# Kernel optimization log

Hardware: AMD Instinct MI355X
Metric: run time of the kernel (lower is better)

The kernel has to match this reference:

```python
import math
import jax, jax.numpy as jnp
import numpy as np

B = 65536
EMBED = 256
COND = 256
TIME = 128
HID = 256
E = 8
RHID = 128
IN_DIM = EMBED + TIME + COND  # 640


def setup_inputs() -> dict:
    key = jax.random.key(0)
    ks = jax.random.split(key, 20)
    s = 0.02
    inp = {
        "z_t": jax.random.normal(ks[0], (B, EMBED), jnp.float32),
        "t": jax.random.uniform(ks[1], (B, 1), jnp.float32),
        "cond": jax.random.normal(ks[2], (B, COND), jnp.float32),
        # time embedding proj (Linear(time,time) -> SiLU -> Linear(time,time))
        "tW1": jax.random.normal(ks[3], (TIME, TIME), jnp.float32) * s,
        "tb1": jnp.zeros((TIME,), jnp.float32),
        "tW2": jax.random.normal(ks[4], (TIME, TIME), jnp.float32) * s,
        "tb2": jnp.zeros((TIME,), jnp.float32),
        # stacked expert weights [E, in, out]
        "eW1": jax.random.normal(ks[5], (E, IN_DIM, HID), jnp.float32) * s,
        "eb1": jnp.zeros((E, HID), jnp.float32),
        "eW2": jax.random.normal(ks[6], (E, HID, HID), jnp.float32) * s,
        "eb2": jnp.zeros((E, HID), jnp.float32),
        "eW3": jax.random.normal(ks[7], (E, HID, EMBED), jnp.float32) * s,
        "eb3": jnp.zeros((E, EMBED), jnp.float32),
        # router
        "rW1": jax.random.normal(ks[8], (IN_DIM, RHID), jnp.float32) * s,
        "rb1": jnp.zeros((RHID,), jnp.float32),
        "rW2": jax.random.normal(ks[9], (RHID, E), jnp.float32) * s,
        "rb2": jnp.zeros((E,), jnp.float32),
    }
    return inp


def _time_embedding(t, tW1, tb1, tW2, tb2):
    half = TIME // 2  # 64
    scale = -math.log(10000.0) / (half - 1)
    freqs = jnp.exp(jnp.arange(half, dtype=t.dtype) * scale)[None, :]  # [1, half]
    angles = t * freqs  # [B, half]
    emb = jnp.concatenate([jnp.sin(angles), jnp.cos(angles)], axis=-1)  # [B, TIME]
    h = jax.nn.silu(emb @ tW1 + tb1)
    return h @ tW2 + tb2


def reference(z_t, t, cond, tW1, tb1, tW2, tb2, eW1, eb1, eW2, eb2, eW3, eb3, rW1, rb1, rW2, rb2):
    time_emb = _time_embedding(t, tW1, tb1, tW2, tb2)
    x = jnp.concatenate([z_t, time_emb, cond], axis=-1)  # [B, IN_DIM]
    # dense MoE: all experts via batched GEMMs (dropout=0 -> identity)
    h1 = jax.nn.silu(jnp.einsum('bi,eih->beh', x, eW1) + eb1)      # [B,E,HID]
    h2 = jax.nn.silu(jnp.einsum('beh,ehk->bek', h1, eW2) + eb2)    # [B,E,HID]
    expert_out = jnp.einsum('beh,ehd->bed', h2, eW3) + eb3         # [B,E,EMBED]
    # router softmax gate
    rh = jax.nn.silu(x @ rW1 + rb1)
    gate = jax.nn.softmax(rh @ rW2 + rb2, axis=-1)                 # [B,E]
    velocity = jnp.einsum('be,bed->bd', gate, expert_out)          # [B,EMBED]
    return velocity, gate
```

## Files before the change

### kernel.cpp

```cpp
#include <hip/hip_runtime.h>

typedef __attribute__((ext_vector_type(8))) short bf16x8;
typedef __attribute__((ext_vector_type(4))) float f32x4;

#define NB_ROWS 65536
#define D_EMBED 256
#define D_HID   256
#define N_EXP   8
#define D_RHID  128
#define D_IN    640
#define D_H1    2048

#define KSTR 72
#define HSTR 264

static __device__ __forceinline__ ushort f2bf(float f) {
  union { float f; unsigned u; } v; v.f = f;
  unsigned r = v.u + 0x7fffu + ((v.u >> 16) & 1u);
  return (ushort)(r >> 16);
}
static __device__ __forceinline__ float bf2f(ushort h) {
  union { unsigned u; float f; } v; v.u = ((unsigned)h) << 16;
  return v.f;
}
static __device__ __forceinline__ float silu_f(float x) {
  return x / (1.0f + __expf(-x));
}

static __device__ __forceinline__ int kswz(int r, int c) {
  return r * 64 + ((((c) >> 3) ^ (r & 7)) << 3) + ((c) & 7);
}

__global__ void prep_transpose(const float* __restrict__ src, ushort* __restrict__ dst,
                               int R, int C, int total) {
  int idx = blockIdx.x * 256 + threadIdx.x;
  if (idx >= total) return;
  int rc = R * C;
  int m = idx / rc;
  int rem = idx - m * rc;
  int r = rem / C;
  int c = rem - r * C;
  dst[m * rc + c * R + r] = f2bf(src[idx]);
}

static __device__ __forceinline__ void stA128s(const ushort* __restrict__ src, int ld,
                                               int kt, ushort* dst, int tid) {
  uint4 v[2];
  #pragma unroll
  for (int c = 0; c < 2; ++c) {
    int f = c * 8192 + tid * 16;
    int r = f >> 7, ce = (f & 127) >> 1;
    v[c] = *(const uint4*)&src[(size_t)r * ld + kt + ce];
  }
  #pragma unroll
  for (int c = 0; c < 2; ++c) {
    int f = c * 8192 + tid * 16;
    int r = f >> 7, ce = (f & 127) >> 1;
    *(uint4*)&dst[kswz(r, ce)] = v[c];
  }
}
static __device__ __forceinline__ void stB256s(const ushort* __restrict__ src, int ld,
                                               int kt, ushort* dst, int tid) {
  uint4 v[4];
  #pragma unroll
  for (int c = 0; c < 4; ++c) {
    int f = c * 8192 + tid * 16;
    int r = f >> 7, ce = (f & 127) >> 1;
    v[c] = *(const uint4*)&src[(size_t)r * ld + kt + ce];
  }
  #pragma unroll
  for (int c = 0; c < 4; ++c) {
    int f = c * 8192 + tid * 16;
    int r = f >> 7, ce = (f & 127) >> 1;
    *(uint4*)&dst[kswz(r, ce)] = v[c];
  }
}
static __device__ __forceinline__ void stageA128_256(const ushort* __restrict__ src, int ld,
                                                     int kt, ushort* dst, int tid) {
  uint4 v[4];
  #pragma unroll
  for (int c = 0; c < 4; ++c) {
    int f = c * 4096 + tid * 16;
    int r = f >> 7, ce = (f & 127) >> 1;
    v[c] = *(const uint4*)&src[(size_t)r * ld + kt + ce];
  }
  #pragma unroll
  for (int c = 0; c < 4; ++c) {
    int f = c * 4096 + tid * 16;
    int r = f >> 7, ce = (f & 127) >> 1;
    *(uint4*)&dst[r * KSTR + ce] = v[c];
  }
}

__global__ __launch_bounds__(512) void time_x_kernel(
    const float* __restrict__ zt, const float* __restrict__ tin,
    const float* __restrict__ cond,
    const ushort* __restrict__ tw1t, const ushort* __restrict__ tw2t,
    const float* __restrict__ tb1, const float* __restrict__ tb2,
    ushort* __restrict__ x) {
  __shared__ __align__(16) ushort sE[128 * 136];
  __shared__ float sFreq[64];
  __shared__ float sB1[128];
  __shared__ float sB2[128];

  const int tid = threadIdx.x;
  const int row0 = blockIdx.x * 128;

  for (int ch = tid; ch < 128 * 64; ch += 512) {
    int r = ch >> 6;
    int c4 = (ch & 63) << 2;
    size_t grow = (size_t)(row0 + r);
    float4 zv = *(const float4*)&zt[grow * 256 + c4];
    ushort4 o; o.x = f2bf(zv.x); o.y = f2bf(zv.y); o.z = f2bf(zv.z); o.w = f2bf(zv.w);
    *(ushort4*)&x[grow * 640 + c4] = o;
    float4 cv = *(const float4*)&cond[grow * 256 + c4];
    ushort4 o2; o2.x = f2bf(cv.x); o2.y = f2bf(cv.y); o2.z = f2bf(cv.z); o2.w = f2bf(cv.w);
    *(ushort4*)&x[grow * 640 + 384 + c4] = o2;
  }

  if (tid < 64) sFreq[tid] = __expf((float)tid * (-9.210340371976184f / 63.0f));
  if (tid < 128) { sB1[tid] = tb1[tid]; sB2[tid] = tb2[tid]; }
  __syncthreads();

  {
    int r = tid >> 2;
    int qd = tid & 3;
    float tv = tin[row0 + r];
    int half = qd >> 1;
    int cbase = (qd & 1) * 32;
    ushort* er = &sE[r * 136 + half * 64 + cbase];
    #pragma unroll
    for (int c = 0; c < 32; ++c) {
      float a = tv * sFreq[cbase + c];
      float v = half ? __cosf(a) : __sinf(a);
      er[c] = f2bf(v);
    }
  }
  __syncthreads();

  const int l = tid & 63;
  const int w = tid >> 6;
  const int wm = w >> 1;
  const int wn = w & 1;
  const int lr = l & 15;
  const int lk = (l >> 4) * 8;
  const int q4 = (l >> 4) * 4;

  f32x4 acc[2][4] = {};
  #pragma unroll
  for (int kk = 0; kk < 4; ++kk) {
    int kb = kk * 32 + lk;
    bf16x8 av[2], bv[4];
    #pragma unroll
    for (int mf = 0; mf < 2; ++mf)
      av[mf] = *(const bf16x8*)&sE[(wm * 32 + mf * 16 + lr) * 136 + kb];
    #pragma unroll
    for (int nf = 0; nf < 4; ++nf)
      bv[nf] = *(const bf16x8*)&tw1t[(size_t)(wn * 64 + nf * 16 + lr) * 128 + kb];
    #pragma unroll
    for (int mf = 0; mf < 2; ++mf)
      #pragma unroll
      for (int nf = 0; nf < 4; ++nf)
        acc[mf][nf] = __builtin_amdgcn_mfma_f32_16x16x32_bf16(av[mf], bv[nf], acc[mf][nf], 0, 0, 0);
  }
  __syncthreads();
  #pragma unroll
  for (int mf = 0; mf < 2; ++mf)
    #pragma unroll
    for (int nf = 0; nf < 4; ++nf) {
      int cc = wn * 64 + nf * 16 + lr;
      #pragma unroll
      for (int rg = 0; rg < 4; ++rg) {
        int rr = wm * 32 + mf * 16 + q4 + rg;
        sE[rr * 136 + cc] = f2bf(silu_f(acc[mf][nf][rg] + sB1[cc]));
      }
    }
  __syncthreads();

  f32x4 acc2[2][4] = {};
  #pragma unroll
  for (int kk = 0; kk < 4; ++kk) {
    int kb = kk * 32 + lk;
    bf16x8 av[2], bv[4];
    #pragma unroll
    for (int mf = 0; mf < 2; ++mf)
      av[mf] = *(const bf16x8*)&sE[(wm * 32 + mf * 16 + lr) * 136 + kb];
    #pragma unroll
    for (int nf = 0; nf < 4; ++nf)
      bv[nf] = *(const bf16x8*)&tw2t[(size_t)(wn * 64 + nf * 16 + lr) * 128 + kb];
    #pragma unroll
    for (int mf = 0; mf < 2; ++mf)
      #pragma unroll
      for (int nf = 0; nf < 4; ++nf)
        acc2[mf][nf] = __builtin_amdgcn_mfma_f32_16x16x32_bf16(av[mf], bv[nf], acc2[mf][nf], 0, 0, 0);
  }
  #pragma unroll
  for (int mf = 0; mf < 2; ++mf)
    #pragma unroll
    for (int nf = 0; nf < 4; ++nf) {
      int cc = wn * 64 + nf * 16 + lr;
      #pragma unroll
      for (int rg = 0; rg < 4; ++rg) {
        int rr = wm * 32 + mf * 16 + q4 + rg;
        x[(size_t)(row0 + rr) * 640 + 256 + cc] = f2bf(acc2[mf][nf][rg] + sB2[cc]);
      }
    }
}

__global__ __launch_bounds__(256) void router_kernel(
    const ushort* __restrict__ xb, const ushort* __restrict__ rw1t,
    const float* __restrict__ rb1, const float* __restrict__ rW2,
    const float* __restrict__ rb2, float* __restrict__ gatef,
    float* __restrict__ gateo) {
  __shared__ __align__(16) ushort smA[128 * KSTR];
  __shared__ __align__(16) ushort smB[128 * KSTR];
  __shared__ __align__(16) ushort rhbuf[128 * 136];
  __shared__ float sW2[128 * 8];

  const int tid = threadIdx.x;
  const int row0 = blockIdx.x * 128;
  for (int i = tid; i < 1024; i += 256) sW2[i] = rW2[i];

  const int l = tid & 63;
  const int w = tid >> 6;
  const int wm = w >> 1, wn = w & 1;
  const int lr = l & 15, lk = (l >> 4) * 8, q4 = (l >> 4) * 4;
  const ushort* xrow = xb + (size_t)row0 * 640;

  f32x4 acc[4][4] = {};
  for (int kt = 0; kt < 640; kt += 64) {
    stageA128_256(xrow, 640, kt, smA, tid);
    stageA128_256(rw1t, 640, kt, smB, tid);
    __syncthreads();
    #pragma unroll
    for (int kk = 0; kk < 2; ++kk) {
      int kb = kk * 32 + lk;
      bf16x8 av[4], bv[4];
      #pragma unroll
      for (int mf = 0; mf < 4; ++mf)
        av[mf] = *(const bf16x8*)&smA[(wm * 64 + mf * 16 + lr) * KSTR + kb];
      #pragma unroll
      for (int nf = 0; nf < 4; ++nf)
        bv[nf] = *(const bf16x8*)&smB[(wn * 64 + nf * 16 + lr) * KSTR + kb];
      #pragma unroll
      for (int mf = 0; mf < 4; ++mf)
        #pragma unroll
        for (int nf = 0; nf < 4; ++nf)
          acc[mf][nf] = __builtin_amdgcn_mfma_f32_16x16x32_bf16(av[mf], bv[nf], acc[mf][nf], 0, 0, 0);
    }
    __syncthreads();
  }
  #pragma unroll
  for (int nf = 0; nf < 4; ++nf) {
    int cc = wn * 64 + nf * 16 + lr;
    float b1v = rb1[cc];
    #pragma unroll
    for (int mf = 0; mf < 4; ++mf)
      #pragma unroll
      for (int rg = 0; rg < 4; ++rg) {
        int rr = wm * 64 + mf * 16 + q4 + rg;
        rhbuf[rr * 136 + cc] = f2bf(silu_f(acc[mf][nf][rg] + b1v));
      }
  }
  __syncthreads();

  if (tid < 128) {
    float a[8];
    #pragma unroll
    for (int e = 0; e < 8; ++e) a[e] = rb2[e];
    #pragma unroll
    for (int i8 = 0; i8 < 16; ++i8) {
      bf16x8 hv = *(const bf16x8*)&rhbuf[tid * 136 + i8 * 8];
      #pragma unroll
      for (int j = 0; j < 8; ++j) {
        float h = bf2f((ushort)hv[j]);
        const float* wrow = &sW2[(i8 * 8 + j) * 8];
        #pragma unroll
        for (int e = 0; e < 8; ++e) a[e] += h * wrow[e];
      }
    }
    float mx = a[0];
    #pragma unroll
    for (int e = 1; e < 8; ++e) mx = fmaxf(mx, a[e]);
    float s = 0.f, ex[8];
    #pragma unroll
    for (int e = 0; e < 8; ++e) { ex[e] = __expf(a[e] - mx); s += ex[e]; }
    float inv = 1.f / s;
    size_t b = (size_t)(row0 + tid);
    #pragma unroll
    for (int e = 0; e < 8; ++e) {
      float g = ex[e] * inv;
      gatef[b * 8 + e] = g;
      gateo[b * 8 + e] = g;
    }
  }
}

__global__ __launch_bounds__(512) void moe_h1_kernel(
    const ushort* __restrict__ xb, const ushort* __restrict__ w1t,
    const float* __restrict__ eb1, ushort* __restrict__ hg) {
  __shared__ __align__(16) ushort smA[128 * 64];
  __shared__ __align__(16) ushort smB[256 * 64];

  const int tid = threadIdx.x;
  int flat = blockIdx.x;
  int sid = (flat & 7) * 512 + (flat >> 3);
  const int rb = sid >> 3;
  const int e  = sid & 7;
  const int row0 = rb * 128;

  const int l = tid & 63;
  const int w = tid >> 6;
  const int wm = w >> 2, wn = w & 3;
  const int lr = l & 15, lk = (l >> 4) * 8, q4 = (l >> 4) * 4;

  const ushort* xrow = xb + (size_t)row0 * 640;
  const ushort* W1 = w1t + (size_t)e * (256 * 640);

  f32x4 acc[4][4] = {};
  for (int kt = 0; kt < 640; kt += 64) {
    stA128s(xrow, 640, kt, smA, tid);
    stB256s(W1, 640, kt, smB, tid);
    __syncthreads();
    #pragma unroll
    for (int kk = 0; kk < 2; ++kk) {
      int kb = kk * 32 + lk;
      bf16x8 av[4], bv[4];
      #pragma unroll
      for (int mf = 0; mf < 4; ++mf)
        av[mf] = *(const bf16x8*)&smA[kswz(wm * 64 + mf * 16 + lr, kb)];
      #pragma unroll
      for (int nf = 0; nf < 4; ++nf)
        bv[nf] = *(const bf16x8*)&smB[kswz(wn * 64 + nf * 16 + lr, kb)];
      #pragma unroll
      for (int mf = 0; mf < 4; ++mf)
        #pragma unroll
        for (int nf = 0; nf < 4; ++nf)
          acc[mf][nf] = __builtin_amdgcn_mfma_f32_16x16x32_bf16(av[mf], bv[nf], acc[mf][nf], 0, 0, 0);
    }
    __syncthreads();
  }
  #pragma unroll
  for (int nf = 0; nf < 4; ++nf) {
    int cc = wn * 64 + nf * 16 + lr;
    float b1v = eb1[e * 256 + cc];
    #pragma unroll
    for (int mf = 0; mf < 4; ++mf)
      #pragma unroll
      for (int rg = 0; rg < 4; ++rg) {
        int rr = wm * 64 + mf * 16 + q4 + rg;
        hg[(size_t)(row0 + rr) * D_H1 + e * 256 + cc] = f2bf(silu_f(acc[mf][nf][rg] + b1v));
      }
  }
}

__global__ __launch_bounds__(512) void moe_h2_kernel(
    ushort* __restrict__ hg, const ushort* __restrict__ w2t,
    const float* __restrict__ eb2, const float* __restrict__ gatef) {
  __shared__ __align__(16) ushort smA[128 * 64];
  __shared__ __align__(16) ushort smB[256 * 64];
  __shared__ float sGate[128];

  const int tid = threadIdx.x;
  int flat = blockIdx.x;
  int sid = (flat & 7) * 512 + (flat >> 3);
  const int rb = sid >> 3;
  const int e  = sid & 7;
  const int row0 = rb * 128;

  const int l = tid & 63;
  const int w = tid >> 6;
  const int wm = w >> 2, wn = w & 3;
  const int lr = l & 15, lk = (l >> 4) * 8, q4 = (l >> 4) * 4;

  if (tid < 128) sGate[tid] = gatef[(size_t)(row0 + tid) * 8 + e];

  ushort* hrow = hg + (size_t)row0 * D_H1 + e * 256;
  const ushort* W2 = w2t + (size_t)e * (256 * 256);

  f32x4 acc[4][4] = {};
  for (int kt = 0; kt < 256; kt += 64) {
    stA128s(hrow, D_H1, kt, smA, tid);
    stB256s(W2, 256, kt, smB, tid);
    __syncthreads();
    #pragma unroll
    for (int kk = 0; kk < 2; ++kk) {
      int kb = kk * 32 + lk;
      bf16x8 av[4], bv[4];
      #pragma unroll
      for (int mf = 0; mf < 4; ++mf)
        av[mf] = *(const bf16x8*)&smA[kswz(wm * 64 + mf * 16 + lr, kb)];
      #pragma unroll
      for (int nf = 0; nf < 4; ++nf)
        bv[nf] = *(const bf16x8*)&smB[kswz(wn * 64 + nf * 16 + lr, kb)];
      #pragma unroll
      for (int mf = 0; mf < 4; ++mf)
        #pragma unroll
        for (int nf = 0; nf < 4; ++nf)
          acc[mf][nf] = __builtin_amdgcn_mfma_f32_16x16x32_bf16(av[mf], bv[nf], acc[mf][nf], 0, 0, 0);
    }
    __syncthreads();
  }
  #pragma unroll
  for (int nf = 0; nf < 4; ++nf) {
    int cc = wn * 64 + nf * 16 + lr;
    float b2v = eb2[e * 256 + cc];
    #pragma unroll
    for (int mf = 0; mf < 4; ++mf)
      #pragma unroll
      for (int rg = 0; rg < 4; ++rg) {
        int rr = wm * 64 + mf * 16 + q4 + rg;
        hrow[(size_t)rr * D_H1 + cc] = f2bf(silu_f(acc[mf][nf][rg] + b2v) * sGate[rr]);
      }
  }
}

__global__ __launch_bounds__(512) void moe_vel_kernel(
    const ushort* __restrict__ hg, const ushort* __restrict__ w3t,
    const float* __restrict__ eb3, const float* __restrict__ gatef,
    float* __restrict__ velout) {
  __shared__ __align__(16) ushort smA[128 * 64];
  __shared__ __align__(16) ushort smB[256 * 64];
  __shared__ float sGate[128 * 8];

  const int tid = threadIdx.x;
  const int row0 = blockIdx.x * 128;
  const int l = tid & 63;
  const int w = tid >> 6;
  const int wm = w >> 2, wn = w & 3;
  const int lr = l & 15, lk = (l >> 4) * 8, q4 = (l >> 4) * 4;

  for (int i = tid; i < 1024; i += 512) sGate[i] = gatef[(size_t)row0 * 8 + i];

  const ushort* hrow = hg + (size_t)row0 * D_H1;
  f32x4 vacc[4][4] = {};
  __syncthreads();

  for (int kt = 0; kt < 2048; kt += 64) {
    const int e = kt >> 8;
    stA128s(hrow, D_H1, kt, smA, tid);
    stB256s(w3t + (size_t)e * (256 * 256), 256, kt & 255, smB, tid);
    __syncthreads();
    #pragma unroll
    for (int kk = 0; kk < 2; ++kk) {
      int kb = kk * 32 + lk;
      bf16x8 av[4], bv[4];
      #pragma unroll
      for (int mf = 0; mf < 4; ++mf)
        av[mf] = *(const bf16x8*)&smA[kswz(wm * 64 + mf * 16 + lr, kb)];
      #pragma unroll
      for (int nf = 0; nf < 4; ++nf)
        bv[nf] = *(const bf16x8*)&smB[kswz(wn * 64 + nf * 16 + lr, kb)];
      #pragma unroll
      for (int mf = 0; mf < 4; ++mf)
        #pragma unroll
        for (int nf = 0; nf < 4; ++nf)
          vacc[mf][nf] = __builtin_amdgcn_mfma_f32_16x16x32_bf16(av[mf], bv[nf], vacc[mf][nf], 0, 0, 0);
    }
    __syncthreads();
  }

  float* eL = (float*)smB;
  for (int i = tid; i < 2048; i += 512) eL[i] = eb3[i];
  __syncthreads();
  #pragma unroll
  for (int mf = 0; mf < 4; ++mf)
    #pragma unroll
    for (int rg = 0; rg < 4; ++rg) {
      int rr = wm * 64 + mf * 16 + q4 + rg;
      const float* gp = &sGate[rr * 8];
      #pragma unroll
      for (int nf = 0; nf < 4; ++nf) {
        int cc = wn * 64 + nf * 16 + lr;
        float bsum = 0.f;
        #pragma unroll
        for (int ee = 0; ee < 8; ++ee) bsum += gp[ee] * eL[ee * 256 + cc];
        velout[(size_t)(row0 + rr) * D_EMBED + cc] = vacc[mf][nf][rg] + bsum;
      }
    }
}

__global__ __launch_bounds__(512) void moe_fused_kernel(
    const ushort* __restrict__ xb, const ushort* __restrict__ w1t,
    const ushort* __restrict__ w2t, const ushort* __restrict__ w3t,
    const float* __restrict__ eb1, const float* __restrict__ eb2,
    const float* __restrict__ eb3, const float* __restrict__ gatef,
    float* __restrict__ velout) {
  __shared__ __align__(16) ushort smA[128 * 64];
  __shared__ __align__(16) ushort smB[256 * 64];
  __shared__ __align__(16) ushort hbuf[128 * HSTR];
  __shared__ float sGate[128 * 8];
  __shared__ float sEb3[8 * 256];

  const int tid = threadIdx.x;
  const int row0 = blockIdx.x * 128;
  const int l = tid & 63;
  const int w = tid >> 6;
  const int wm = w >> 2, wn = w & 3;
  const int lr = l & 15, lk = (l >> 4) * 8, q4 = (l >> 4) * 4;

  for (int i = tid; i < 1024; i += 512) sGate[i] = gatef[(size_t)row0 * 8 + i];
  for (int i = tid; i < 2048; i += 512) sEb3[i] = eb3[i];

  const ushort* xrow = xb + (size_t)row0 * 640;
  f32x4 vacc[4][4] = {};
  __syncthreads();

  for (int e = 0; e < 8; ++e) {
    const ushort* W1 = w1t + (size_t)e * (256 * 640);
    const ushort* W2 = w2t + (size_t)e * (256 * 256);
    const ushort* W3 = w3t + (size_t)e * (256 * 256);

    f32x4 acc[4][4] = {};
    for (int kt = 0; kt < 640; kt += 64) {
      stA128s(xrow, 640, kt, smA, tid);
      stB256s(W1, 640, kt, smB, tid);
      __syncthreads();
      #pragma unroll
      for (int kk = 0; kk < 2; ++kk) {
        int kb = kk * 32 + lk;
        bf16x8 av[4], bv[4];
        #pragma unroll
        for (int mf = 0; mf < 4; ++mf)
          av[mf] = *(const bf16x8*)&smA[kswz(wm * 64 + mf * 16 + lr, kb)];
        #pragma unroll
        for (int nf = 0; nf < 4; ++nf)
          bv[nf] = *(const bf16x8*)&smB[kswz(wn * 64 + nf * 16 + lr, kb)];
        #pragma unroll
        for (int mf = 0; mf < 4; ++mf)
          #pragma unroll
          for (int nf = 0; nf < 4; ++nf)
            acc[mf][nf] = __builtin_amdgcn_mfma_f32_16x16x32_bf16(av[mf], bv[nf], acc[mf][nf], 0, 0, 0);
      }
      __syncthreads();
    }
    #pragma unroll
    for (int nf = 0; nf < 4; ++nf) {
      int cc = wn * 64 + nf * 16 + lr;
      float b1v = eb1[e * 256 + cc];
      #pragma unroll
      for (int mf = 0; mf < 4; ++mf)
        #pragma unroll
        for (int rg = 0; rg < 4; ++rg) {
          int rr = wm * 64 + mf * 16 + q4 + rg;
          hbuf[rr * HSTR + cc] = f2bf(silu_f(acc[mf][nf][rg] + b1v));
        }
    }
    __syncthreads();

    #pragma unroll
    for (int mf = 0; mf < 4; ++mf)
      #pragma unroll
      for (int nf = 0; nf < 4; ++nf)
        acc[mf][nf] = (f32x4){0.f, 0.f, 0.f, 0.f};
    for (int kt = 0; kt < 256; kt += 64) {
      stB256s(W2, 256, kt, smB, tid);
      __syncthreads();
      #pragma unroll
      for (int kk = 0; kk < 2; ++kk) {
        int kbl = kk * 32 + lk;
        int kbh = kt + kbl;
        bf16x8 av[4], bv[4];
        #pragma unroll
        for (int mf = 0; mf < 4; ++mf)
          av[mf] = *(const bf16x8*)&hbuf[(wm * 64 + mf * 16 + lr) * HSTR + kbh];
        #pragma unroll
        for (int nf = 0; nf < 4; ++nf)
          bv[nf] = *(const bf16x8*)&smB[kswz(wn * 64 + nf * 16 + lr, kbl)];
        #pragma unroll
        for (int mf = 0; mf < 4; ++mf)
          #pragma unroll
          for (int nf = 0; nf < 4; ++nf)
            acc[mf][nf] = __builtin_amdgcn_mfma_f32_16x16x32_bf16(av[mf], bv[nf], acc[mf][nf], 0, 0, 0);
      }
      __syncthreads();
    }
    #pragma unroll
    for (int nf = 0; nf < 4; ++nf) {
      int cc = wn * 64 + nf * 16 + lr;
      float b2v = eb2[e * 256 + cc];
      #pragma unroll
      for (int mf = 0; mf < 4; ++mf)
        #pragma unroll
        for (int rg = 0; rg < 4; ++rg) {
          int rr = wm * 64 + mf * 16 + q4 + rg;
          float gv = sGate[rr * 8 + e];
          hbuf[rr * HSTR + cc] = f2bf(silu_f(acc[mf][nf][rg] + b2v) * gv);
        }
    }
    __syncthreads();

    for (int kt = 0; kt < 256; kt += 64) {
      stB256s(W3, 256, kt, smB, tid);
      __syncthreads();
      #pragma unroll
      for (int kk = 0; kk < 2; ++kk) {
        int kbl = kk * 32 + lk;
        int kbh = kt + kbl;
        bf16x8 av[4], bv[4];
        #pragma unroll
        for (int mf = 0; mf < 4; ++mf)
          av[mf] = *(const bf16x8*)&hbuf[(wm * 64 + mf * 16 + lr) * HSTR + kbh];
        #pragma unroll
        for (int nf = 0; nf < 4; ++nf)
          bv[nf] = *(const bf16x8*)&smB[kswz(wn * 64 + nf * 16 + lr, kbl)];
        #pragma unroll
        for (int mf = 0; mf < 4; ++mf)
          #pragma unroll
          for (int nf = 0; nf < 4; ++nf)
            vacc[mf][nf] = __builtin_amdgcn_mfma_f32_16x16x32_bf16(av[mf], bv[nf], vacc[mf][nf], 0, 0, 0);
      }
      __syncthreads();
    }
  }

  #pragma unroll
  for (int mf = 0; mf < 4; ++mf)
    #pragma unroll
    for (int rg = 0; rg < 4; ++rg) {
      int rr = wm * 64 + mf * 16 + q4 + rg;
      const float* gp = &sGate[rr * 8];
      #pragma unroll
      for (int nf = 0; nf < 4; ++nf) {
        int cc = wn * 64 + nf * 16 + lr;
        float bsum = 0.f;
        #pragma unroll
        for (int ee = 0; ee < 8; ++ee) bsum += gp[ee] * sEb3[ee * 256 + cc];
        velout[(size_t)(row0 + rr) * D_EMBED + cc] = vacc[mf][nf][rg] + bsum;
      }
    }
}

extern "C" void kernel_launch(void* const* d_in, const int* in_sizes, int n_in,
                              void* d_out, int out_size, void* d_ws, size_t ws_size,
                              hipStream_t stream) {
  const float* zt   = (const float*)d_in[0];
  const float* tin  = (const float*)d_in[1];
  const float* cond = (const float*)d_in[2];
  const float* tW1  = (const float*)d_in[3];
  const float* tb1  = (const float*)d_in[4];
  const float* tW2  = (const float*)d_in[5];
  const float* tb2  = (const float*)d_in[6];
  const float* eW1  = (const float*)d_in[7];
  const float* eb1  = (const float*)d_in[8];
  const float* eW2  = (const float*)d_in[9];
  const float* eb2  = (const float*)d_in[10];
  const float* eW3  = (const float*)d_in[11];
  const float* eb3  = (const float*)d_in[12];
  const float* rW1  = (const float*)d_in[13];
  const float* rb1  = (const float*)d_in[14];
  const float* rW2  = (const float*)d_in[15];
  const float* rb2  = (const float*)d_in[16];

  char* wp = (char*)d_ws;
  ushort* xb    = (ushort*)wp; wp += (size_t)NB_ROWS * D_IN * 2;
  float*  gatef = (float*)wp;  wp += (size_t)NB_ROWS * 8 * 4;
  ushort* w1t   = (ushort*)wp; wp += (size_t)N_EXP * D_HID * D_IN * 2;
  ushort* w2t   = (ushort*)wp; wp += (size_t)N_EXP * D_HID * D_HID * 2;
  ushort* w3t   = (ushort*)wp; wp += (size_t)N_EXP * D_HID * D_EMBED * 2;
  ushort* rw1t  = (ushort*)wp; wp += (size_t)D_RHID * D_IN * 2;
  ushort* tw1t  = (ushort*)wp; wp += (size_t)128 * 128 * 2;
  ushort* tw2t  = (ushort*)wp; wp += (size_t)128 * 128 * 2;
  ushort* hg    = (ushort*)wp; wp += (size_t)NB_ROWS * D_H1 * 2;
  size_t need_big = (size_t)(wp - (char*)d_ws);

  float* velout  = (float*)d_out;
  float* gateout = velout + (size_t)NB_ROWS * D_EMBED;

  {
    int tot;
    tot = 128 * 128;
    prep_transpose<<<(tot + 255) / 256, 256, 0, stream>>>(tW1, tw1t, 128, 128, tot);
    prep_transpose<<<(tot + 255) / 256, 256, 0, stream>>>(tW2, tw2t, 128, 128, tot);
    tot = D_IN * D_RHID;
    prep_transpose<<<(tot + 255) / 256, 256, 0, stream>>>(rW1, rw1t, D_IN, D_RHID, tot);
    tot = N_EXP * D_IN * D_HID;
    prep_transpose<<<(tot + 255) / 256, 256, 0, stream>>>(eW1, w1t, D_IN, D_HID, tot);
    tot = N_EXP * D_HID * D_HID;
    prep_transpose<<<(tot + 255) / 256, 256, 0, stream>>>(eW2, w2t, D_HID, D_HID, tot);
    tot = N_EXP * D_HID * D_EMBED;
    prep_transpose<<<(tot + 255) / 256, 256, 0, stream>>>(eW3, w3t, D_HID, D_EMBED, tot);
  }

  time_x_kernel<<<512, 512, 0, stream>>>(zt, tin, cond, tw1t, tw2t, tb1, tb2, xb);
  router_kernel<<<512, 256, 0, stream>>>(xb, rw1t, rb1, rW2, rb2, gatef, gateout);

  if (ws_size >= need_big) {
    moe_h1_kernel<<<4096, 512, 0, stream>>>(xb, w1t, eb1, hg);
    moe_h2_kernel<<<4096, 512, 0, stream>>>(hg, w2t, eb2, gatef);
    moe_vel_kernel<<<512, 512, 0, stream>>>(hg, w3t, eb3, gatef, velout);
  } else {
    moe_fused_kernel<<<512, 512, 0, stream>>>(xb, w1t, w2t, w3t,
                                              eb1, eb2, eb3, gatef, velout);
  }
}
```

Before: 660.1 us.

## Chunk MoE rows to fit workspace and retile velocity kernel to 64x128

The three-kernel MoE path now processes rows in chunks sized to the available workspace, so the intermediate hidden buffer can shrink and stay closer to cache rather than needing the full batch allocation. The velocity kernel is retiled from 128x256 tiles with 512 threads to 64x128 tiles with 256 threads, giving four times as many workgroups so more CUs are busy during the long K=2048 reduction. Each workgroup in that kernel now rereads the A tile for both column halves, adding some traffic, and chunking adds kernel launches.

```diff
diff --git a/kernel.cpp b/kernel.cpp
--- a/kernel.cpp
+++ b/kernel.cpp
@@ -75,6 +75,38 @@
     *(uint4*)&dst[kswz(r, ce)] = v[c];
   }
 }
+static __device__ __forceinline__ void stA64_256s(const ushort* __restrict__ src, int ld,
+                                                  int kt, ushort* dst, int tid) {
+  uint4 v[2];
+  #pragma unroll
+  for (int c = 0; c < 2; ++c) {
+    int f = c * 4096 + tid * 16;
+    int r = f >> 7, ce = (f & 127) >> 1;
+    v[c] = *(const uint4*)&src[(size_t)r * ld + kt + ce];
+  }
+  #pragma unroll
+  for (int c = 0; c < 2; ++c) {
+    int f = c * 4096 + tid * 16;
+    int r = f >> 7, ce = (f & 127) >> 1;
+    *(uint4*)&dst[kswz(r, ce)] = v[c];
+  }
+}
+static __device__ __forceinline__ void stB128_256s(const ushort* __restrict__ src, int ld,
+                                                   int kt, ushort* dst, int tid) {
+  uint4 v[4];
+  #pragma unroll
+  for (int c = 0; c < 4; ++c) {
+    int f = c * 4096 + tid * 16;
+    int r = f >> 7, ce = (f & 127) >> 1;
+    v[c] = *(const uint4*)&src[(size_t)r * ld + kt + ce];
+  }
+  #pragma unroll
+  for (int c = 0; c < 4; ++c) {
+    int f = c * 4096 + tid * 16;
+    int r = f >> 7, ce = (f & 127) >> 1;
+    *(uint4*)&dst[kswz(r, ce)] = v[c];
+  }
+}
 static __device__ __forceinline__ void stageA128_256(const ushort* __restrict__ src, int ld,
                                                      int kt, ushort* dst, int tid) {
   uint4 v[4];
@@ -298,23 +330,24 @@
 
 __global__ __launch_bounds__(512) void moe_h1_kernel(
     const ushort* __restrict__ xb, const ushort* __restrict__ w1t,
-    const float* __restrict__ eb1, ushort* __restrict__ hg) {
+    const float* __restrict__ eb1, ushort* __restrict__ hg, int row_base) {
   __shared__ __align__(16) ushort smA[128 * 64];
   __shared__ __align__(16) ushort smB[256 * 64];
 
   const int tid = threadIdx.x;
+  int nwg = gridDim.x;
   int flat = blockIdx.x;
-  int sid = (flat & 7) * 512 + (flat >> 3);
+  int sid = (flat & 7) * (nwg >> 3) + (flat >> 3);
   const int rb = sid >> 3;
   const int e  = sid & 7;
-  const int row0 = rb * 128;
+  const int lrow0 = rb * 128;
 
   const int l = tid & 63;
   const int w = tid >> 6;
   const int wm = w >> 2, wn = w & 3;
   const int lr = l & 15, lk = (l >> 4) * 8, q4 = (l >> 4) * 4;
 
-  const ushort* xrow = xb + (size_t)row0 * 640;
+  const ushort* xrow = xb + (size_t)(row_base + lrow0) * 640;
   const ushort* W1 = w1t + (size_t)e * (256 * 640);
 
   f32x4 acc[4][4] = {};
@@ -349,33 +382,34 @@
       #pragma unroll
       for (int rg = 0; rg < 4; ++rg) {
         int rr = wm * 64 + mf * 16 + q4 + rg;
-        hg[(size_t)(row0 + rr) * D_H1 + e * 256 + cc] = f2bf(silu_f(acc[mf][nf][rg] + b1v));
+        hg[(size_t)(lrow0 + rr) * D_H1 + e * 256 + cc] = f2bf(silu_f(acc[mf][nf][rg] + b1v));
       }
   }
 }
 
 __global__ __launch_bounds__(512) void moe_h2_kernel(
     ushort* __restrict__ hg, const ushort* __restrict__ w2t,
-    const float* __restrict__ eb2, const float* __restrict__ gatef) {
+    const float* __restrict__ eb2, const float* __restrict__ gatef, int row_base) {
   __shared__ __align__(16) ushort smA[128 * 64];
   __shared__ __align__(16) ushort smB[256 * 64];
   __shared__ float sGate[128];
 
   const int tid = threadIdx.x;
+  int nwg = gridDim.x;
   int flat = blockIdx.x;
-  int sid = (flat & 7) * 512 + (flat >> 3);
+  int sid = (flat & 7) * (nwg >> 3) + (flat >> 3);
   const int rb = sid >> 3;
   const int e  = sid & 7;
-  const int row0 = rb * 128;
+  const int lrow0 = rb * 128;
 
   const int l = tid & 63;
   const int w = tid >> 6;
   const int wm = w >> 2, wn = w & 3;
   const int lr = l & 15, lk = (l >> 4) * 8, q4 = (l >> 4) * 4;
 
-  if (tid < 128) sGate[tid] = gatef[(size_t)(row0 + tid) * 8 + e];
-
-  ushort* hrow = hg + (size_t)row0 * D_H1 + e * 256;
+  if (tid < 128) sGate[tid] = gatef[(size_t)(row_base + lrow0 + tid) * 8 + e];
+
+  ushort* hrow = hg + (size_t)lrow0 * D_H1 + e * 256;
   const ushort* W2 = w2t + (size_t)e * (256 * 256);
 
   f32x4 acc[4][4] = {};
@@ -415,44 +449,56 @@
   }
 }
 
-__global__ __launch_bounds__(512) void moe_vel_kernel(
+__global__ __launch_bounds__(256) void moe_vel_kernel(
     const ushort* __restrict__ hg, const ushort* __restrict__ w3t,
     const float* __restrict__ eb3, const float* __restrict__ gatef,
-    float* __restrict__ velout) {
-  __shared__ __align__(16) ushort smA[128 * 64];
-  __shared__ __align__(16) ushort smB[256 * 64];
-  __shared__ float sGate[128 * 8];
+    float* __restrict__ velout, int row_base) {
+  __shared__ __align__(16) ushort smA[64 * 64];
+  __shared__ __align__(16) ushort smB[128 * 64];
+  __shared__ float sGate[64 * 8];
+  __shared__ float sEb3[8 * 128];
 
   const int tid = threadIdx.x;
-  const int row0 = blockIdx.x * 128;
+  int nwg = gridDim.x;
+  int flat = blockIdx.x;
+  int sid = (flat & 7) * (nwg >> 3) + (flat >> 3);
+  const int rb = sid >> 1;
+  const int nb = sid & 1;
+  const int lrow0 = rb * 64;
+  const int col0 = nb * 128;
+
   const int l = tid & 63;
   const int w = tid >> 6;
-  const int wm = w >> 2, wn = w & 3;
+  const int wm = w >> 1, wn = w & 1;
   const int lr = l & 15, lk = (l >> 4) * 8, q4 = (l >> 4) * 4;
 
-  for (int i = tid; i < 1024; i += 512) sGate[i] = gatef[(size_t)row0 * 8 + i];
-
-  const ushort* hrow = hg + (size_t)row0 * D_H1;
-  f32x4 vacc[4][4] = {};
+  for (int i = tid; i < 512; i += 256) sGate[i] = gatef[(size_t)(row_base + lrow0) * 8 + i];
+  for (int i = tid; i < 1024; i += 256) {
+    int ee = i >> 7, c = i & 127;
+    sEb3[i] = eb3[ee * 256 + col0 + c];
+  }
+
+  const ushort* hrow = hg + (size_t)lrow0 * D_H1;
+  f32x4 vacc[2][4] = {};
   __syncthreads();
 
   for (int kt = 0; kt < 2048; kt += 64) {
     const int e = kt >> 8;
-    stA128s(hrow, D_H1, kt, smA, tid);
-    stB256s(w3t + (size_t)e * (256 * 256), 256, kt & 255, smB, tid);
+    stA64_256s(hrow, D_H1, kt, smA, tid);
+    stB128_256s(w3t + (size_t)e * (256 * 256) + (size_t)col0 * 256, 256, kt & 255, smB, tid);
     __syncthreads();
     #pragma unroll
     for (int kk = 0; kk < 2; ++kk) {
       int kb = kk * 32 + lk;
-      bf16x8 av[4], bv[4];
-      #pragma unroll
-      for (int mf = 0; mf < 4; ++mf)
-        av[mf] = *(const bf16x8*)&smA[kswz(wm * 64 + mf * 16 + lr, kb)];
+      bf16x8 av[2], bv[4];
+      #pragma unroll
+      for (int mf = 0; mf < 2; ++mf)
+        av[mf] = *(const bf16x8*)&smA[kswz(wm * 32 + mf * 16 + lr, kb)];
       #pragma unroll
       for (int nf = 0; nf < 4; ++nf)
         bv[nf] = *(const bf16x8*)&smB[kswz(wn * 64 + nf * 16 + lr, kb)];
       #pragma unroll
-      for (int mf = 0; mf < 4; ++mf)
+      for (int mf = 0; mf < 2; ++mf)
         #pragma unroll
         for (int nf = 0; nf < 4; ++nf)
           vacc[mf][nf] = __builtin_amdgcn_mfma_f32_16x16x32_bf16(av[mf], bv[nf], vacc[mf][nf], 0, 0, 0);
@@ -460,22 +506,19 @@
     __syncthreads();
   }
 
-  float* eL = (float*)smB;
-  for (int i = tid; i < 2048; i += 512) eL[i] = eb3[i];
-  __syncthreads();
-  #pragma unroll
-  for (int mf = 0; mf < 4; ++mf)
+  #pragma unroll
+  for (int mf = 0; mf < 2; ++mf)
     #pragma unroll
     for (int rg = 0; rg < 4; ++rg) {
-      int rr = wm * 64 + mf * 16 + q4 + rg;
+      int rr = wm * 32 + mf * 16 + q4 + rg;
       const float* gp = &sGate[rr * 8];
       #pragma unroll
       for (int nf = 0; nf < 4; ++nf) {
         int cc = wn * 64 + nf * 16 + lr;
         float bsum = 0.f;
         #pragma unroll
-        for (int ee = 0; ee < 8; ++ee) bsum += gp[ee] * eL[ee * 256 + cc];
-        velout[(size_t)(row0 + rr) * D_EMBED + cc] = vacc[mf][nf][rg] + bsum;
+        for (int ee = 0; ee < 8; ++ee) bsum += gp[ee] * sEb3[ee * 128 + cc];
+        velout[(size_t)(row_base + lrow0 + rr) * D_EMBED + col0 + cc] = vacc[mf][nf][rg] + bsum;
       }
     }
 }
@@ -661,8 +704,13 @@
   ushort* rw1t  = (ushort*)wp; wp += (size_t)D_RHID * D_IN * 2;
   ushort* tw1t  = (ushort*)wp; wp += (size_t)128 * 128 * 2;
   ushort* tw2t  = (ushort*)wp; wp += (size_t)128 * 128 * 2;
-  ushort* hg    = (ushort*)wp; wp += (size_t)NB_ROWS * D_H1 * 2;
-  size_t need_big = (size_t)(wp - (char*)d_ws);
+  ushort* hg    = (ushort*)wp;
+  size_t base = (size_t)(wp - (char*)d_ws);
+
+  int CH = 0;
+  for (int cand = NB_ROWS; cand >= 8192; cand >>= 1) {
+    if (base + (size_t)cand * D_H1 * 2 <= ws_size) { CH = cand; break; }
+  }
 
   float* velout  = (float*)d_out;
   float* gateout = velout + (size_t)NB_ROWS * D_EMBED;
@@ -685,10 +733,12 @@
   time_x_kernel<<<512, 512, 0, stream>>>(zt, tin, cond, tw1t, tw2t, tb1, tb2, xb);
   router_kernel<<<512, 256, 0, stream>>>(xb, rw1t, rb1, rW2, rb2, gatef, gateout);
 
-  if (ws_size >= need_big) {
-    moe_h1_kernel<<<4096, 512, 0, stream>>>(xb, w1t, eb1, hg);
-    moe_h2_kernel<<<4096, 512, 0, stream>>>(hg, w2t, eb2, gatef);
-    moe_vel_kernel<<<512, 512, 0, stream>>>(hg, w3t, eb3, gatef, velout);
+  if (CH > 0) {
+    for (int r0 = 0; r0 < NB_ROWS; r0 += CH) {
+      moe_h1_kernel<<<(CH / 128) * 8, 512, 0, stream>>>(xb, w1t, eb1, hg, r0);
+      moe_h2_kernel<<<(CH / 128) * 8, 512, 0, stream>>>(hg, w2t, eb2, gatef, r0);
+      moe_vel_kernel<<<(CH / 64) * 2, 256, 0, stream>>>(hg, w3t, eb3, gatef, velout, r0);
+    }
   } else {
     moe_fused_kernel<<<512, 512, 0, stream>>>(xb, w1t, w2t, w3t,
                                               eb1, eb2, eb3, gatef, velout);
```

After: 670.8 us. Within noise of the previous version (+1.6%).

## Load expert weights via direct global-to-LDS with pre-swizzled layout; chunk rows

Applied to the files above, without the earlier changes.

Expert weight matrices are now pre-swizzled during the transpose prep so the B tiles can be copied straight into LDS with global_load_lds, skipping the register round trip in the split h1/h2/vel kernels. The row dimension is split into chunks sized to the available workspace, so the intermediate hidden buffer can be smaller, and the vel kernel gains a block-index remap. The fused fallback switches to a linear LDS store to match the new weight layout. This relies on the swizzle produced by the prep step matching the one used for reads, and adds extra launches when chunking is needed.

```diff
diff --git a/kernel.cpp b/kernel.cpp
--- a/kernel.cpp
+++ b/kernel.cpp
@@ -42,7 +42,31 @@
   int c = rem - r * C;
   dst[m * rc + c * R + r] = f2bf(src[idx]);
 }
-
+__global__ void prep_transpose_swz(const float* __restrict__ src, ushort* __restrict__ dst,
+                                   int R, int C, int total) {
+  int idx = blockIdx.x * 256 + threadIdx.x;
+  if (idx >= total) return;
+  int rc = R * C;
+  int m = idx / rc;
+  int rem = idx - m * rc;
+  int r = rem / C;
+  int c = rem - r * C;
+  int p = (r & ~63) + (((((r >> 3) & 7) ^ (c & 7)) << 3) | (r & 7));
+  dst[m * rc + c * R + p] = f2bf(src[idx]);
+}
+
+static __device__ __forceinline__ void glB256_512(const ushort* __restrict__ src, int ld,
+                                                  int kt, ushort* dst, int tid, int w) {
+  #pragma unroll
+  for (int c = 0; c < 4; ++c) {
+    int f = c * 8192 + tid * 16;
+    int r = f >> 7, ce = (f & 127) >> 1;
+    __builtin_amdgcn_global_load_lds(
+        (const __attribute__((address_space(1))) void*)(src + (size_t)r * ld + kt + ce),
+        (__attribute__((address_space(3))) void*)(dst + ((c * 8192 + w * 1024) >> 1)),
+        16, 0, 0);
+  }
+}
 static __device__ __forceinline__ void stA128s(const ushort* __restrict__ src, int ld,
                                                int kt, ushort* dst, int tid) {
   uint4 v[2];
@@ -59,8 +83,8 @@
     *(uint4*)&dst[kswz(r, ce)] = v[c];
   }
 }
-static __device__ __forceinline__ void stB256s(const ushort* __restrict__ src, int ld,
-                                               int kt, ushort* dst, int tid) {
+static __device__ __forceinline__ void stB256lin(const ushort* __restrict__ src, int ld,
+                                                 int kt, ushort* dst, int tid) {
   uint4 v[4];
   #pragma unroll
   for (int c = 0; c < 4; ++c) {
@@ -72,7 +96,7 @@
   for (int c = 0; c < 4; ++c) {
     int f = c * 8192 + tid * 16;
     int r = f >> 7, ce = (f & 127) >> 1;
-    *(uint4*)&dst[kswz(r, ce)] = v[c];
+    *(uint4*)&dst[r * 64 + ce] = v[c];
   }
 }
 static __device__ __forceinline__ void stageA128_256(const ushort* __restrict__ src, int ld,
@@ -298,29 +322,30 @@
 
 __global__ __launch_bounds__(512) void moe_h1_kernel(
     const ushort* __restrict__ xb, const ushort* __restrict__ w1t,
-    const float* __restrict__ eb1, ushort* __restrict__ hg) {
+    const float* __restrict__ eb1, ushort* __restrict__ hg, int row_base) {
   __shared__ __align__(16) ushort smA[128 * 64];
   __shared__ __align__(16) ushort smB[256 * 64];
 
   const int tid = threadIdx.x;
+  int nwg = gridDim.x;
   int flat = blockIdx.x;
-  int sid = (flat & 7) * 512 + (flat >> 3);
+  int sid = (flat & 7) * (nwg >> 3) + (flat >> 3);
   const int rb = sid >> 3;
   const int e  = sid & 7;
-  const int row0 = rb * 128;
+  const int lrow0 = rb * 128;
 
   const int l = tid & 63;
   const int w = tid >> 6;
   const int wm = w >> 2, wn = w & 3;
   const int lr = l & 15, lk = (l >> 4) * 8, q4 = (l >> 4) * 4;
 
-  const ushort* xrow = xb + (size_t)row0 * 640;
+  const ushort* xrow = xb + (size_t)(row_base + lrow0) * 640;
   const ushort* W1 = w1t + (size_t)e * (256 * 640);
 
   f32x4 acc[4][4] = {};
   for (int kt = 0; kt < 640; kt += 64) {
     stA128s(xrow, 640, kt, smA, tid);
-    stB256s(W1, 640, kt, smB, tid);
+    glB256_512(W1, 640, kt, smB, tid, w);
     __syncthreads();
     #pragma unroll
     for (int kk = 0; kk < 2; ++kk) {
@@ -349,39 +374,40 @@
       #pragma unroll
       for (int rg = 0; rg < 4; ++rg) {
         int rr = wm * 64 + mf * 16 + q4 + rg;
-        hg[(size_t)(row0 + rr) * D_H1 + e * 256 + cc] = f2bf(silu_f(acc[mf][nf][rg] + b1v));
+        hg[(size_t)(lrow0 + rr) * D_H1 + e * 256 + cc] = f2bf(silu_f(acc[mf][nf][rg] + b1v));
       }
   }
 }
 
 __global__ __launch_bounds__(512) void moe_h2_kernel(
     ushort* __restrict__ hg, const ushort* __restrict__ w2t,
-    const float* __restrict__ eb2, const float* __restrict__ gatef) {
+    const float* __restrict__ eb2, const float* __restrict__ gatef, int row_base) {
   __shared__ __align__(16) ushort smA[128 * 64];
   __shared__ __align__(16) ushort smB[256 * 64];
   __shared__ float sGate[128];
 
   const int tid = threadIdx.x;
+  int nwg = gridDim.x;
   int flat = blockIdx.x;
-  int sid = (flat & 7) * 512 + (flat >> 3);
+  int sid = (flat & 7) * (nwg >> 3) + (flat >> 3);
   const int rb = sid >> 3;
   const int e  = sid & 7;
-  const int row0 = rb * 128;
+  const int lrow0 = rb * 128;
 
   const int l = tid & 63;
   const int w = tid >> 6;
   const int wm = w >> 2, wn = w & 3;
   const int lr = l & 15, lk = (l >> 4) * 8, q4 = (l >> 4) * 4;
 
-  if (tid < 128) sGate[tid] = gatef[(size_t)(row0 + tid) * 8 + e];
-
-  ushort* hrow = hg + (size_t)row0 * D_H1 + e * 256;
+  if (tid < 128) sGate[tid] = gatef[(size_t)(row_base + lrow0 + tid) * 8 + e];
+
+  ushort* hrow = hg + (size_t)lrow0 * D_H1 + e * 256;
   const ushort* W2 = w2t + (size_t)e * (256 * 256);
 
   f32x4 acc[4][4] = {};
   for (int kt = 0; kt < 256; kt += 64) {
     stA128s(hrow, D_H1, kt, smA, tid);
-    stB256s(W2, 256, kt, smB, tid);
+    glB256_512(W2, 256, kt, smB, tid, w);
     __syncthreads();
     #pragma unroll
     for (int kk = 0; kk < 2; ++kk) {
@@ -418,28 +444,32 @@
 __global__ __launch_bounds__(512) void moe_vel_kernel(
     const ushort* __restrict__ hg, const ushort* __restrict__ w3t,
     const float* __restrict__ eb3, const float* __restrict__ gatef,
-    float* __restrict__ velout) {
+    float* __restrict__ velout, int row_base) {
   __shared__ __align__(16) ushort smA[128 * 64];
   __shared__ __align__(16) ushort smB[256 * 64];
   __shared__ float sGate[128 * 8];
 
   const int tid = threadIdx.x;
-  const int row0 = blockIdx.x * 128;
+  int nwg = gridDim.x;
+  int flat = blockIdx.x;
+  int sid = (flat & 7) * (nwg >> 3) + (flat >> 3);
+  const int lrow0 = sid * 128;
+
   const int l = tid & 63;
   const int w = tid >> 6;
   const int wm = w >> 2, wn = w & 3;
   const int lr = l & 15, lk = (l >> 4) * 8, q4 = (l >> 4) * 4;
 
-  for (int i = tid; i < 1024; i += 512) sGate[i] = gatef[(size_t)row0 * 8 + i];
-
-  const ushort* hrow = hg + (size_t)row0 * D_H1;
+  for (int i = tid; i < 1024; i += 512) sGate[i] = gatef[(size_t)(row_base + lrow0) * 8 + i];
+
+  const ushort* hrow = hg + (size_t)lrow0 * D_H1;
   f32x4 vacc[4][4] = {};
   __syncthreads();
 
   for (int kt = 0; kt < 2048; kt += 64) {
     const int e = kt >> 8;
     stA128s(hrow, D_H1, kt, smA, tid);
-    stB256s(w3t + (size_t)e * (256 * 256), 256, kt & 255, smB, tid);
+    glB256_512(w3t + (size_t)e * (256 * 256), 256, kt & 255, smB, tid, w);
     __syncthreads();
     #pragma unroll
     for (int kk = 0; kk < 2; ++kk) {
@@ -475,7 +505,7 @@
         float bsum = 0.f;
         #pragma unroll
         for (int ee = 0; ee < 8; ++ee) bsum += gp[ee] * eL[ee * 256 + cc];
-        velout[(size_t)(row0 + rr) * D_EMBED + cc] = vacc[mf][nf][rg] + bsum;
+        velout[(size_t)(row_base + lrow0 + rr) * D_EMBED + cc] = vacc[mf][nf][rg] + bsum;
       }
     }
 }
@@ -514,7 +544,7 @@
     f32x4 acc[4][4] = {};
     for (int kt = 0; kt < 640; kt += 64) {
       stA128s(xrow, 640, kt, smA, tid);
-      stB256s(W1, 640, kt, smB, tid);
+      stB256lin(W1, 640, kt, smB, tid);
       __syncthreads();
       #pragma unroll
       for (int kk = 0; kk < 2; ++kk) {
@@ -554,7 +584,7 @@
       for (int nf = 0; nf < 4; ++nf)
         acc[mf][nf] = (f32x4){0.f, 0.f, 0.f, 0.f};
     for (int kt = 0; kt < 256; kt += 64) {
-      stB256s(W2, 256, kt, smB, tid);
+      stB256lin(W2, 256, kt, smB, tid);
       __syncthreads();
       #pragma unroll
       for (int kk = 0; kk < 2; ++kk) {
@@ -591,7 +621,7 @@
     __syncthreads();
 
     for (int kt = 0; kt < 256; kt += 64) {
-      stB256s(W3, 256, kt, smB, tid);
+      stB256lin(W3, 256, kt, smB, tid);
       __syncthreads();
       #pragma unroll
       for (int kk = 0; kk < 2; ++kk) {
@@ -661,8 +691,13 @@
   ushort* rw1t  = (ushort*)wp; wp += (size_t)D_RHID * D_IN * 2;
   ushort* tw1t  = (ushort*)wp; wp += (size_t)128 * 128 * 2;
   ushort* tw2t  = (ushort*)wp; wp += (size_t)128 * 128 * 2;
-  ushort* hg    = (ushort*)wp; wp += (size_t)NB_ROWS * D_H1 * 2;
-  size_t need_big = (size_t)(wp - (char*)d_ws);
+  ushort* hg    = (ushort*)wp;
+  size_t base = (size_t)(wp - (char*)d_ws);
+
+  int CH = 0;
+  for (int cand = NB_ROWS; cand >= 8192; cand >>= 1) {
+    if (base + (size_t)cand * D_H1 * 2 <= ws_size) { CH = cand; break; }
+  }
 
   float* velout  = (float*)d_out;
   float* gateout = velout + (size_t)NB_ROWS * D_EMBED;
@@ -675,20 +710,22 @@
     tot = D_IN * D_RHID;
     prep_transpose<<<(tot + 255) / 256, 256, 0, stream>>>(rW1, rw1t, D_IN, D_RHID, tot);
     tot = N_EXP * D_IN * D_HID;
-    prep_transpose<<<(tot + 255) / 256, 256, 0, stream>>>(eW1, w1t, D_IN, D_HID, tot);
+    prep_transpose_swz<<<(tot + 255) / 256, 256, 0, stream>>>(eW1, w1t, D_IN, D_HID, tot);
     tot = N_EXP * D_HID * D_HID;
-    prep_transpose<<<(tot + 255) / 256, 256, 0, stream>>>(eW2, w2t, D_HID, D_HID, tot);
+    prep_transpose_swz<<<(tot + 255) / 256, 256, 0, stream>>>(eW2, w2t, D_HID, D_HID, tot);
     tot = N_EXP * D_HID * D_EMBED;
-    prep_transpose<<<(tot + 255) / 256, 256, 0, stream>>>(eW3, w3t, D_HID, D_EMBED, tot);
+    prep_transpose_swz<<<(tot + 255) / 256, 256, 0, stream>>>(eW3, w3t, D_HID, D_EMBED, tot);
   }
 
   time_x_kernel<<<512, 512, 0, stream>>>(zt, tin, cond, tw1t, tw2t, tb1, tb2, xb);
   router_kernel<<<512, 256, 0, stream>>>(xb, rw1t, rb1, rW2, rb2, gatef, gateout);
 
-  if (ws_size >= need_big) {
-    moe_h1_kernel<<<4096, 512, 0, stream>>>(xb, w1t, eb1, hg);
-    moe_h2_kernel<<<4096, 512, 0, stream>>>(hg, w2t, eb2, gatef);
-    moe_vel_kernel<<<512, 512, 0, stream>>>(hg, w3t, eb3, gatef, velout);
+  if (CH > 0) {
+    for (int r0 = 0; r0 < NB_ROWS; r0 += CH) {
+      moe_h1_kernel<<<(CH / 128) * 8, 512, 0, stream>>>(xb, w1t, eb1, hg, r0);
+      moe_h2_kernel<<<(CH / 128) * 8, 512, 0, stream>>>(hg, w2t, eb2, gatef, r0);
+      moe_vel_kernel<<<CH / 128, 512, 0, stream>>>(hg, w3t, eb3, gatef, velout, r0);
+    }
   } else {
     moe_fused_kernel<<<512, 512, 0, stream>>>(xb, w1t, w2t, w3t,
                                               eb1, eb2, eb3, gatef, velout);
```

After: 649.1 us. Within noise of the previous version (-1.7%).
